# Optimization experiments

Hardware: AMD Instinct MI355X
Metric: run time of the kernel (lower is better)

The kernel has to match this reference:

```python
import jax, jax.numpy as jnp
import numpy as np

N, K, D, H, F = 4, 2048, 512, 8, 2048
Dh = D // H  # per-head dim_q = dim_v = dim_out = 64
EPS = 1e-10


def _uinit(k, shape, fan_sum):
    c = (6.0 / fan_sum) ** 0.5
    return jax.random.uniform(k, shape, jnp.float32, -c, c)


def setup_inputs() -> dict:
    key = jax.random.key(0)
    ks = jax.random.split(key, 8)
    x = jax.random.normal(ks[0], (N, K, D), jnp.float32)
    # per-head projection weights, stacked over heads: (H, D, Dh)
    Wq = _uinit(ks[1], (H, D, Dh), D + Dh)
    Wk = _uinit(ks[2], (H, D, Dh), D + Dh)
    Wv = _uinit(ks[3], (H, D, Dh), D + Dh)
    bq = jnp.zeros((H, Dh), jnp.float32)
    bk = jnp.zeros((H, Dh), jnp.float32)
    bv = jnp.zeros((H, Dh), jnp.float32)
    Wo = _uinit(ks[4], (H * Dh, D), H * Dh + D)
    bo = jnp.zeros((D,), jnp.float32)
    W1 = _uinit(ks[5], (D, F), D + F)
    b1 = jnp.zeros((F,), jnp.float32)
    W2 = _uinit(ks[6], (F, D), F + D)
    b2 = jnp.zeros((D,), jnp.float32)
    g1 = jnp.ones((D,), jnp.float32)
    be1 = jnp.zeros((D,), jnp.float32)
    g2 = jnp.ones((D,), jnp.float32)
    be2 = jnp.zeros((D,), jnp.float32)
    # causal mask: True = masked position (masked_fill semantics)
    mask = jnp.broadcast_to(jnp.triu(jnp.ones((K, K), bool), 1), (N, K, K))
    return dict(x=x, Wq=Wq, bq=bq, Wk=Wk, bk=bk, Wv=Wv, bv=bv, Wo=Wo, bo=bo,
                W1=W1, b1=b1, W2=W2, b2=b2, g1=g1, be1=be1, g2=g2, be2=be2,
                mask=mask)


def _layer_norm(x, g, b):
    m = x.mean(-1, keepdims=True)
    v = ((x - m) ** 2).mean(-1, keepdims=True)
    return g * (x - m) / jnp.sqrt(v + EPS) + b


def _block(x, Wq, bq, Wk, bk, Wv, bv, Wo, bo, W1, b1, W2, b2, g1, be1, g2, be2, mask):
    # per-head projections: (N, H, K, Dh)
    q = jnp.einsum('nkd,hde->nhke', x, Wq) + bq[None, :, None, :]
    k = jnp.einsum('nkd,hde->nhke', x, Wk) + bk[None, :, None, :]
    v = jnp.einsum('nkd,hde->nhke', x, Wv) + bv[None, :, None, :]
    # full score matrix (N, H, K, K) -- faithful to bmm-softmax-bmm
    s = jnp.einsum('nhqe,nhke->nhqk', q, k) / (Dh ** 0.5)
    s = jnp.where(mask[:, None], -1e9, s)
    w = jax.nn.softmax(s, axis=-1)
    att = jnp.einsum('nhqk,nhke->nhqe', w, v)
    att = att.transpose(0, 2, 1, 3).reshape(N, K, H * Dh)  # concat heads
    att = att @ Wo + bo
    h1 = _layer_norm(x + att, g1, be1)
    ff = jax.nn.relu(h1 @ W1 + b1) @ W2 + b2
    return _layer_norm(h1 + ff, g2, be2)


def reference(x, Wq, bq, Wk, bk, Wv, bv, Wo, bo, W1, b1, W2, b2, g1, be1, g2, be2, mask):
    return _block(x, Wq, bq, Wk, bk, Wv, bv, Wo, bo, W1, b1, W2, b2, g1, be1, g2, be2, mask)
```

## Files before the change

kernel.cpp:

```cpp
#include <hip/hip_runtime.h>
#include <cstdint>

typedef unsigned short u16;
typedef __bf16 bf16x8 __attribute__((ext_vector_type(8)));
typedef float f32x4 __attribute__((ext_vector_type(4)));
struct __align__(8) U2 { unsigned x, y; };

#define NEG_INF (-__builtin_inff())

__device__ __forceinline__ u16 f2bf(float f) {
  unsigned u = __builtin_bit_cast(unsigned, f);
  u += 0x7FFFu + ((u >> 16) & 1u);
  return (u16)(u >> 16);
}
__device__ __forceinline__ u16 bfbits(__bf16 x) { return __builtin_bit_cast(u16, x); }
__device__ __forceinline__ unsigned pk2(float a, float b) {
  u16 lo = bfbits((__bf16)a), hi = bfbits((__bf16)b);
  return (unsigned)lo | ((unsigned)hi << 16);
}

__device__ __forceinline__ void async16(u16* dst, const u16* src) {
  __builtin_amdgcn_global_load_lds(
      (__attribute__((address_space(1))) void*)(u16*)src,
      (__attribute__((address_space(3))) void*)dst, 16, 0, 0);
}

__global__ __launch_bounds__(256) void k_cvt(const float4* __restrict__ in,
                                             uint4* __restrict__ out, int n8) {
  int i = blockIdx.x * 256 + threadIdx.x;
  if (i >= n8) return;
  float4 a = in[2 * i], b = in[2 * i + 1];
  uint4 r;
  r.x = (unsigned)f2bf(a.x) | ((unsigned)f2bf(a.y) << 16);
  r.y = (unsigned)f2bf(a.z) | ((unsigned)f2bf(a.w) << 16);
  r.z = (unsigned)f2bf(b.x) | ((unsigned)f2bf(b.y) << 16);
  r.w = (unsigned)f2bf(b.z) | ((unsigned)f2bf(b.w) << 16);
  out[i] = r;
}

__global__ __launch_bounds__(256) void k_transpose(const float* __restrict__ in,
                                                   u16* __restrict__ out, int R, int C) {
  __shared__ float t[32][65];
  int b = blockIdx.z;
  int r0 = blockIdx.y * 32, c0 = blockIdx.x * 64;
  const float* ip = in + (size_t)b * R * C;
  u16* op = out + (size_t)b * R * C;
  int tx = threadIdx.x & 63, ty = threadIdx.x >> 6;
#pragma unroll
  for (int i = 0; i < 32; i += 4) {
    int r = r0 + ty + i, c = c0 + tx;
    t[ty + i][tx] = (r < R && c < C) ? ip[(size_t)r * C + c] : 0.f;
  }
  __syncthreads();
  int cx = threadIdx.x & 31, cy = threadIdx.x >> 5;
#pragma unroll
  for (int j = 0; j < 64; j += 8) {
    int oc = c0 + cy + j, orr = r0 + cx;
    if (oc < C && orr < R) op[(size_t)oc * R + orr] = f2bf(t[cx][cy + j]);
  }
}

__global__ __launch_bounds__(256) void k_transpose_qkv(const float* __restrict__ Wq,
                                                       const float* __restrict__ Wk,
                                                       const float* __restrict__ Wv,
                                                       u16* __restrict__ out) {
  __shared__ float t[32][65];
  int z = blockIdx.z;
  const float* W = (z < 8) ? Wq : (z < 16) ? Wk : Wv;
  const float* ip = W + (size_t)(z & 7) * 32768;
  u16* op = out + (size_t)z * 32768;
  int r0 = blockIdx.y * 32;
  int tx = threadIdx.x & 63, ty = threadIdx.x >> 6;
#pragma unroll
  for (int i = 0; i < 32; i += 4)
    t[ty + i][tx] = ip[(size_t)(r0 + ty + i) * 64 + tx];
  __syncthreads();
  int cx = threadIdx.x & 31, cy = threadIdx.x >> 5;
#pragma unroll
  for (int j = 0; j < 64; j += 8)
    op[(size_t)(cy + j) * 512 + r0 + cx] = f2bf(t[cx][cy + j]);
}

__global__ __launch_bounds__(256) void k_pack_bias(const float* __restrict__ bq,
                                                   const float* __restrict__ bk,
                                                   const float* __restrict__ bv,
                                                   float* __restrict__ bpk) {
  int i = blockIdx.x * 256 + threadIdx.x;
  if (i < 1536) {
    int m = i >> 9, r = i & 511;
    const float* B = (m == 0) ? bq : (m == 1) ? bk : bv;
    bpk[i] = B[r];
  }
}

template <int EPI, int BN>
__global__ __launch_bounds__(256) void k_gemm(const u16* __restrict__ A,
                                              const u16* __restrict__ BT,
                                              const float* __restrict__ bias,
                                              void* __restrict__ Cout,
                                              int M, int N, int Kd) {
  constexpr int HALF = 8192 + BN * 64;
  __shared__ __align__(16) u16 lds[2 * HALF];
  constexpr int NFR = BN / 32;
  constexpr int BITER = BN / 32;
  const int tid = threadIdx.x, wid = tid >> 6, lane = tid & 63;
  const int lr = lane & 15, lg = lane >> 4;
  const int wr = wid >> 1, wc = wid & 1;
  const int tm = blockIdx.x * 128, tn = blockIdx.y * BN;

  f32x4 acc[4][NFR] = {};

  const int srow = lane >> 3;
  const int kb = (lane & 7) ^ srow;

  auto STAGE = [&](int buf, int kt) {
    u16* base = lds + buf * HALF;
#pragma unroll
    for (int it = 0; it < 4; ++it) {
      int rid = wid * 4 + it;
      int row = rid * 8 + srow;
      async16(base + rid * 512, A + (size_t)(tm + row) * Kd + kt + kb * 8);
    }
#pragma unroll
    for (int it = 0; it < BITER; ++it) {
      int rid = wid * BITER + it;
      int row = rid * 8 + srow;
      async16(base + 8192 + rid * 512, BT + (size_t)(tn + row) * Kd + kt + kb * 8);
    }
  };

  const int nkt = Kd >> 6;
  STAGE(0, 0);
  __syncthreads();

  for (int ki = 0; ki < nkt; ++ki) {
    if (ki + 1 < nkt) STAGE((ki + 1) & 1, (ki + 1) << 6);
    const char* lp = (const char*)(lds + (ki & 1) * HALF);
#pragma unroll
    for (int ks = 0; ks < 2; ++ks) {
      const int kbyte = ks * 64 + lg * 16;
      bf16x8 af[4], bfr[NFR];
#pragma unroll
      for (int mi = 0; mi < 4; ++mi) {
        int row = wr * 64 + mi * 16 + lr;
        af[mi] = *(const bf16x8*)(lp + row * 128 + (kbyte ^ ((row & 7) << 4)));
      }
#pragma unroll
      for (int nj = 0; nj < NFR; ++nj) {
        int row = wc * (BN / 2) + nj * 16 + lr;
        bfr[nj] = *(const bf16x8*)(lp + 16384 + row * 128 + (kbyte ^ ((row & 7) << 4)));
      }
#pragma unroll
      for (int mi = 0; mi < 4; ++mi)
#pragma unroll
        for (int nj = 0; nj < NFR; ++nj)
          acc[mi][nj] = __builtin_amdgcn_mfma_f32_16x16x32_bf16(af[mi], bfr[nj], acc[mi][nj], 0, 0, 0);
    }
    __syncthreads();
  }

#pragma unroll
  for (int mi = 0; mi < 4; ++mi)
#pragma unroll
    for (int nj = 0; nj < NFR; ++nj) {
      int col = tn + wc * (BN / 2) + nj * 16 + lr;
      float bv = bias[col];
#pragma unroll
      for (int r = 0; r < 4; ++r) {
        int row = tm + wr * 64 + mi * 16 + lg * 4 + r;
        float v = acc[mi][nj][r] + bv;
        if (EPI == 1) v = v > 0.f ? v : 0.f;
        if (EPI == 2)
          ((float*)Cout)[(size_t)row * N + col] = v;
        else
          ((u16*)Cout)[(size_t)row * N + col] = f2bf(v);
      }
    }
}

__global__ __launch_bounds__(256) void k_attn(const u16* __restrict__ QKV,
                                              u16* __restrict__ att) {
  __shared__ __align__(16) u16 lds[36864];
  const int lin = blockIdx.x;
  const int L = (lin & 7) * 64 + (lin >> 3);
  const int p = L & 15, nh = L >> 4;
  const int n = nh >> 3, h = nh & 7;
  const int tid = threadIdx.x, wid = tid >> 6, lane = tid & 63;
  const int lr = lane & 15, lg = lane >> 4;
  char* lp = (char*)lds;
  const u16* Qp = QKV + (size_t)(n * 2048) * 1536 + h * 64;
  const u16* Kp = Qp + 512;
  const u16* Vp = Qp + 1024;

  const int vkv = (tid & 31) * 2;
  const int vd0 = (tid >> 5) * 8;
  const int pwb = 65536 + wid * 2048;
  const float C2 = 0.18033688011112042f;
  const float B0 = 14.426950408889634f;

  for (int ph = 0; ph < 2; ++ph) {
    const int qc = (ph == 0) ? p : 31 - p;
    const int ntiles = qc + 1;
    const int qw = qc * 64 + wid * 16;
    const int qa = qw + lr;

    bf16x8 qf[2];
#pragma unroll
    for (int ks = 0; ks < 2; ++ks)
      qf[ks] = *(const bf16x8*)(Qp + (size_t)(qw + lr) * 1536 + ks * 32 + lg * 8);

    f32x4 o[4] = {};
    float lpart = 0.f;

    auto STAGE_K = [&](int t, int b) {
      const int kv0 = t * 64;
#pragma unroll
      for (int it = 0; it < 2; ++it) {
        int c = (wid * 2 + it) * 64 + lane;
        int row = c >> 3, ce = ((c & 7) ^ (row & 7)) * 8;
        async16(&lds[b * 4096 + (wid * 2 + it) * 512],
                Kp + (size_t)(kv0 + row) * 1536 + ce);
      }
    };
    auto VLAND = [&](bf16x8 va, bf16x8 vb, int b) {
#pragma unroll
      for (int jj = 0; jj < 8; ++jj) {
        int d = vd0 + jj;
        unsigned pk = (unsigned)bfbits(va[jj]) | ((unsigned)bfbits(vb[jj]) << 16);
        *(unsigned*)(lp + 32768 + b * 8192 + d * 128 + ((vkv * 2) ^ ((d & 7) << 4))) = pk;
      }
    };
    auto COMPUTE = [&](int t, int b) {
      const int kv0 = t * 64;
      f32x4 s[4] = {};
      __builtin_amdgcn_s_setprio(1);
#pragma unroll
      for (int nj = 0; nj < 4; ++nj) {
        int row = nj * 16 + lr;
#pragma unroll
        for (int ks = 0; ks < 2; ++ks) {
          bf16x8 kf = *(const bf16x8*)(lp + b * 8192 + row * 128 +
                                       ((ks * 64 + lg * 16) ^ ((row & 7) << 4)));
          s[nj] = __builtin_amdgcn_mfma_f32_16x16x32_bf16(kf, qf[ks], s[nj], 0, 0, 0);
        }
      }
      __builtin_amdgcn_s_setprio(0);

      if (t == ntiles - 1) {
#pragma unroll
        for (int nj = 0; nj < 4; ++nj) {
          int kvb = kv0 + nj * 16 + lg * 4;
#pragma unroll
          for (int r = 0; r < 4; ++r)
            if (kvb + r > qa) s[nj][r] = NEG_INF;
        }
      }

      float psum = 0.f;
#pragma unroll
      for (int nj = 0; nj < 4; ++nj)
#pragma unroll
        for (int r = 0; r < 4; ++r) {
          float pv = exp2f(fmaf(s[nj][r], C2, -B0));
          s[nj][r] = pv;
          psum += pv;
        }
      lpart += psum;

#pragma unroll
      for (int nj = 0; nj < 4; ++nj) {
        U2 val;
        val.x = pk2(s[nj][0], s[nj][1]);
        val.y = pk2(s[nj][2], s[nj][3]);
        *(U2*)(lp + pwb + lr * 128 + ((nj * 32 + lg * 8) ^ ((lr & 7) << 4))) = val;
      }

      bf16x8 pa[2];
#pragma unroll
      for (int ks = 0; ks < 2; ++ks)
        pa[ks] = *(const bf16x8*)(lp + pwb + lr * 128 +
                                  ((ks * 64 + lg * 16) ^ ((lr & 7) << 4)));
      __builtin_amdgcn_s_setprio(1);
#pragma unroll
      for (int nd = 0; nd < 4; ++nd) {
        int row = nd * 16 + lr;
#pragma unroll
        for (int ks = 0; ks < 2; ++ks) {
          bf16x8 vf = *(const bf16x8*)(lp + 32768 + b * 8192 + row * 128 +
                                       ((ks * 64 + lg * 16) ^ ((row & 7) << 4)));
          o[nd] = __builtin_amdgcn_mfma_f32_16x16x32_bf16(vf, pa[ks], o[nd], 0, 0, 0);
        }
      }
      __builtin_amdgcn_s_setprio(0);
    };

    STAGE_K(0, 0);
    if (ntiles > 1) STAGE_K(1, 1);
    {
      bf16x8 v0 = *(const bf16x8*)(Vp + (size_t)vkv * 1536 + vd0);
      bf16x8 v1 = *(const bf16x8*)(Vp + (size_t)(vkv + 1) * 1536 + vd0);
      VLAND(v0, v1, 0);
      if (ntiles > 1) {
        bf16x8 v2 = *(const bf16x8*)(Vp + (size_t)(64 + vkv) * 1536 + vd0);
        bf16x8 v3 = *(const bf16x8*)(Vp + (size_t)(64 + vkv + 1) * 1536 + vd0);
        VLAND(v2, v3, 1);
      }
    }
    __syncthreads();

    for (int t = 0; t < ntiles; t += 2) {
      const bool pre0 = (t + 2 < ntiles);
      const bool pre1 = (t + 3 < ntiles);
      bf16x8 va0, vb0, va1, vb1;
      if (pre0) {
        STAGE_K(t + 2, (t + 2) & 3);
        va0 = *(const bf16x8*)(Vp + (size_t)((t + 2) * 64 + vkv) * 1536 + vd0);
        vb0 = *(const bf16x8*)(Vp + (size_t)((t + 2) * 64 + vkv + 1) * 1536 + vd0);
      }
      if (pre1) {
        STAGE_K(t + 3, (t + 3) & 3);
        va1 = *(const bf16x8*)(Vp + (size_t)((t + 3) * 64 + vkv) * 1536 + vd0);
        vb1 = *(const bf16x8*)(Vp + (size_t)((t + 3) * 64 + vkv + 1) * 1536 + vd0);
      }

      COMPUTE(t, t & 3);
      if (t + 1 < ntiles) COMPUTE(t + 1, (t + 1) & 3);

      if (pre0) VLAND(va0, vb0, (t + 2) & 3);
      if (pre1) VLAND(va1, vb1, (t + 3) & 3);
      __syncthreads();
    }

    float lsum = lpart;
    lsum += __shfl_xor(lsum, 16);
    lsum += __shfl_xor(lsum, 32);
    float li = 1.0f / lsum;

    u16* ap = att + (size_t)(n * 2048 + qw + lr) * 512 + h * 64 + lg * 4;
#pragma unroll
    for (int nd = 0; nd < 4; ++nd) {
      U2 val;
      val.x = pk2(o[nd][0] * li, o[nd][1] * li);
      val.y = pk2(o[nd][2] * li, o[nd][3] * li);
      *(U2*)(ap + nd * 16) = val;
    }
  }
}

__global__ __launch_bounds__(256) void k_add_ln(const float* __restrict__ X,
                                                const float* __restrict__ Y,
                                                const float* __restrict__ gam,
                                                const float* __restrict__ bet,
                                                float* __restrict__ outf,
                                                u16* __restrict__ outb) {
  const int wid = threadIdx.x >> 6, lane = threadIdx.x & 63;
  const size_t row = (size_t)blockIdx.x * 4 + wid;
  const float4* x = (const float4*)(X + row * 512);
  const float4* y = (const float4*)(Y + row * 512);
  float4 a0 = x[lane], a1 = x[lane + 64];
  float4 b0 = y[lane], b1 = y[lane + 64];
  float v[8];
  v[0] = a0.x + b0.x; v[1] = a0.y + b0.y; v[2] = a0.z + b0.z; v[3] = a0.w + b0.w;
  v[4] = a1.x + b1.x; v[5] = a1.y + b1.y; v[6] = a1.z + b1.z; v[7] = a1.w + b1.w;
  float s = 0.f, ss = 0.f;
#pragma unroll
  for (int i = 0; i < 8; ++i) { s += v[i]; ss += v[i] * v[i]; }
#pragma unroll
  for (int m = 1; m < 64; m <<= 1) { s += __shfl_xor(s, m); ss += __shfl_xor(ss, m); }
  float mean = s * (1.f / 512.f);
  float var = ss * (1.f / 512.f) - mean * mean;
  float rstd = rsqrtf(var + 1e-10f);
  float4 g0 = ((const float4*)gam)[lane], g1 = ((const float4*)gam)[lane + 64];
  float4 e0 = ((const float4*)bet)[lane], e1 = ((const float4*)bet)[lane + 64];
  float o[8];
  o[0] = g0.x * (v[0] - mean) * rstd + e0.x;
  o[1] = g0.y * (v[1] - mean) * rstd + e0.y;
  o[2] = g0.z * (v[2] - mean) * rstd + e0.z;
  o[3] = g0.w * (v[3] - mean) * rstd + e0.w;
  o[4] = g1.x * (v[4] - mean) * rstd + e1.x;
  o[5] = g1.y * (v[5] - mean) * rstd + e1.y;
  o[6] = g1.z * (v[6] - mean) * rstd + e1.z;
  o[7] = g1.w * (v[7] - mean) * rstd + e1.w;
  float4* of = (float4*)(outf + row * 512);
  float4 w0, w1;
  w0.x = o[0]; w0.y = o[1]; w0.z = o[2]; w0.w = o[3];
  w1.x = o[4]; w1.y = o[5]; w1.z = o[6]; w1.w = o[7];
  of[lane] = w0;
  of[lane + 64] = w1;
  if (outb) {
    u16* ob = outb + row * 512;
    U2 p0, p1;
    p0.x = pk2(o[0], o[1]); p0.y = pk2(o[2], o[3]);
    p1.x = pk2(o[4], o[5]); p1.y = pk2(o[6], o[7]);
    *(U2*)(ob + lane * 4) = p0;
    *(U2*)(ob + 256 + lane * 4) = p1;
  }
}

extern "C" void kernel_launch(void* const* d_in, const int* in_sizes, int n_in,
                              void* d_out, int out_size, void* d_ws, size_t ws_size,
                              hipStream_t stream) {
  const float* x  = (const float*)d_in[0];
  const float* Wq = (const float*)d_in[1];
  const float* bq = (const float*)d_in[2];
  const float* Wk = (const float*)d_in[3];
  const float* bk = (const float*)d_in[4];
  const float* Wv = (const float*)d_in[5];
  const float* bv = (const float*)d_in[6];
  const float* Wo = (const float*)d_in[7];
  const float* bo = (const float*)d_in[8];
  const float* W1 = (const float*)d_in[9];
  const float* b1 = (const float*)d_in[10];
  const float* W2 = (const float*)d_in[11];
  const float* b2 = (const float*)d_in[12];
  const float* g1 = (const float*)d_in[13];
  const float* be1 = (const float*)d_in[14];
  const float* g2 = (const float*)d_in[15];
  const float* be2 = (const float*)d_in[16];

  char* ws = (char*)d_ws;
  u16* xb   = (u16*)(ws + 0);
  u16* attb = (u16*)(ws + 0);
  u16* h1b  = (u16*)(ws + 0);
  u16* WqkvT = (u16*)(ws + (size_t)(8u << 20));
  u16* WoT = WqkvT + 786432;
  u16* W1T = WoT + 262144;
  u16* W2T = W1T + 1048576;
  float* bqkv = (float*)(W2T + 1048576);
  u16* QKV = (u16*)(ws + (size_t)(16u << 20));
  float* attproj = (float*)(ws + (size_t)(16u << 20));
  u16* ff1 = (u16*)(ws + (size_t)(16u << 20));
  float* ffn2 = (float*)(ws + (size_t)(50u << 20));
  float* h1f = (float*)d_out;

  k_cvt<<<2048, 256, 0, stream>>>((const float4*)x, (uint4*)xb, 524288);
  k_transpose_qkv<<<dim3(1, 16, 24), 256, 0, stream>>>(Wq, Wk, Wv, WqkvT);
  k_transpose<<<dim3(8, 16, 1), 256, 0, stream>>>(Wo, WoT, 512, 512);
  k_transpose<<<dim3(32, 16, 1), 256, 0, stream>>>(W1, W1T, 512, 2048);
  k_transpose<<<dim3(8, 64, 1), 256, 0, stream>>>(W2, W2T, 2048, 512);
  k_pack_bias<<<6, 256, 0, stream>>>(bq, bk, bv, bqkv);

  k_gemm<0, 128><<<dim3(64, 12), 256, 0, stream>>>(xb, WqkvT, bqkv, QKV, 8192, 1536, 512);
  k_attn<<<512, 256, 0, stream>>>(QKV, attb);
  k_gemm<2, 64><<<dim3(64, 8), 256, 0, stream>>>(attb, WoT, bo, attproj, 8192, 512, 512);
  k_add_ln<<<2048, 256, 0, stream>>>(x, attproj, g1, be1, h1f, h1b);
  k_gemm<1, 128><<<dim3(64, 16), 256, 0, stream>>>(h1b, W1T, b1, ff1, 8192, 2048, 512);
  k_gemm<2, 64><<<dim3(64, 8), 256, 0, stream>>>(ff1, W2T, b2, ffn2, 8192, 512, 2048);
  k_add_ln<<<2048, 256, 0, stream>>>(h1f, ffn2, g2, be2, (float*)d_out, nullptr);
}
```

Before: 179.1 us.

## Store GEMM residual outputs in bf16 and remap GEMM blocks for XCD locality

The Wo and W2 GEMMs now write bf16 instead of fp32 outputs, and the add+layernorm kernels read those bf16 values and widen them. This halves the write and read traffic of the two intermediate tensors, at a small cost in precision before the layer norm. GEMM grids become 1D, with block ids remapped so that the blocks landing on the same XCD cover a contiguous group of 8 M-tiles, which aims to improve L2 reuse of the A rows.

```diff
diff --git a/kernel.cpp b/kernel.cpp
--- a/kernel.cpp
+++ b/kernel.cpp
@@ -12,6 +12,10 @@
   unsigned u = __builtin_bit_cast(unsigned, f);
   u += 0x7FFFu + ((u >> 16) & 1u);
   return (u16)(u >> 16);
+}
+__device__ __forceinline__ float bf2f(u16 b) {
+  unsigned u = (unsigned)b << 16;
+  return __builtin_bit_cast(float, u);
 }
 __device__ __forceinline__ u16 bfbits(__bf16 x) { return __builtin_bit_cast(u16, x); }
 __device__ __forceinline__ unsigned pk2(float a, float b) {
@@ -97,7 +101,7 @@
 __global__ __launch_bounds__(256) void k_gemm(const u16* __restrict__ A,
                                               const u16* __restrict__ BT,
                                               const float* __restrict__ bias,
-                                              void* __restrict__ Cout,
+                                              u16* __restrict__ Cout,
                                               int M, int N, int Kd) {
   constexpr int HALF = 8192 + BN * 64;
   __shared__ __align__(16) u16 lds[2 * HALF];
@@ -106,7 +110,10 @@
   const int tid = threadIdx.x, wid = tid >> 6, lane = tid & 63;
   const int lr = lane & 15, lg = lane >> 4;
   const int wr = wid >> 1, wc = wid & 1;
-  const int tm = blockIdx.x * 128, tn = blockIdx.y * BN;
+  const int bid = blockIdx.x;
+  const int xcd = bid & 7, local = bid >> 3;
+  const int tm = (xcd * 8 + (local & 7)) * 128;
+  const int tn = (local >> 3) * BN;
 
   f32x4 acc[4][NFR] = {};
 
@@ -170,10 +177,7 @@
         int row = tm + wr * 64 + mi * 16 + lg * 4 + r;
         float v = acc[mi][nj][r] + bv;
         if (EPI == 1) v = v > 0.f ? v : 0.f;
-        if (EPI == 2)
-          ((float*)Cout)[(size_t)row * N + col] = v;
-        else
-          ((u16*)Cout)[(size_t)row * N + col] = f2bf(v);
+        Cout[(size_t)row * N + col] = f2bf(v);
       }
     }
 }
@@ -348,7 +352,7 @@
 }
 
 __global__ __launch_bounds__(256) void k_add_ln(const float* __restrict__ X,
-                                                const float* __restrict__ Y,
+                                                const u16* __restrict__ Yb,
                                                 const float* __restrict__ gam,
                                                 const float* __restrict__ bet,
                                                 float* __restrict__ outf,
@@ -356,12 +360,18 @@
   const int wid = threadIdx.x >> 6, lane = threadIdx.x & 63;
   const size_t row = (size_t)blockIdx.x * 4 + wid;
   const float4* x = (const float4*)(X + row * 512);
-  const float4* y = (const float4*)(Y + row * 512);
   float4 a0 = x[lane], a1 = x[lane + 64];
-  float4 b0 = y[lane], b1 = y[lane + 64];
+  U2 y0 = *(const U2*)(Yb + row * 512 + lane * 4);
+  U2 y1 = *(const U2*)(Yb + row * 512 + 256 + lane * 4);
   float v[8];
-  v[0] = a0.x + b0.x; v[1] = a0.y + b0.y; v[2] = a0.z + b0.z; v[3] = a0.w + b0.w;
-  v[4] = a1.x + b1.x; v[5] = a1.y + b1.y; v[6] = a1.z + b1.z; v[7] = a1.w + b1.w;
+  v[0] = a0.x + bf2f((u16)(y0.x & 0xFFFF));
+  v[1] = a0.y + bf2f((u16)(y0.x >> 16));
+  v[2] = a0.z + bf2f((u16)(y0.y & 0xFFFF));
+  v[3] = a0.w + bf2f((u16)(y0.y >> 16));
+  v[4] = a1.x + bf2f((u16)(y1.x & 0xFFFF));
+  v[5] = a1.y + bf2f((u16)(y1.x >> 16));
+  v[6] = a1.z + bf2f((u16)(y1.y & 0xFFFF));
+  v[7] = a1.w + bf2f((u16)(y1.y >> 16));
   float s = 0.f, ss = 0.f;
 #pragma unroll
   for (int i = 0; i < 8; ++i) { s += v[i]; ss += v[i] * v[i]; }
@@ -428,9 +438,9 @@
   u16* W2T = W1T + 1048576;
   float* bqkv = (float*)(W2T + 1048576);
   u16* QKV = (u16*)(ws + (size_t)(16u << 20));
-  float* attproj = (float*)(ws + (size_t)(16u << 20));
+  u16* attproj = (u16*)(ws + (size_t)(16u << 20));
   u16* ff1 = (u16*)(ws + (size_t)(16u << 20));
-  float* ffn2 = (float*)(ws + (size_t)(50u << 20));
+  u16* ffn2 = (u16*)(ws + (size_t)(50u << 20));
   float* h1f = (float*)d_out;
 
   k_cvt<<<2048, 256, 0, stream>>>((const float4*)x, (uint4*)xb, 524288);
@@ -440,11 +450,11 @@
   k_transpose<<<dim3(8, 64, 1), 256, 0, stream>>>(W2, W2T, 2048, 512);
   k_pack_bias<<<6, 256, 0, stream>>>(bq, bk, bv, bqkv);
 
-  k_gemm<0, 128><<<dim3(64, 12), 256, 0, stream>>>(xb, WqkvT, bqkv, QKV, 8192, 1536, 512);
+  k_gemm<0, 128><<<768, 256, 0, stream>>>(xb, WqkvT, bqkv, QKV, 8192, 1536, 512);
   k_attn<<<512, 256, 0, stream>>>(QKV, attb);
-  k_gemm<2, 64><<<dim3(64, 8), 256, 0, stream>>>(attb, WoT, bo, attproj, 8192, 512, 512);
+  k_gemm<0, 64><<<512, 256, 0, stream>>>(attb, WoT, bo, attproj, 8192, 512, 512);
   k_add_ln<<<2048, 256, 0, stream>>>(x, attproj, g1, be1, h1f, h1b);
-  k_gemm<1, 128><<<dim3(64, 16), 256, 0, stream>>>(h1b, W1T, b1, ff1, 8192, 2048, 512);
-  k_gemm<2, 64><<<dim3(64, 8), 256, 0, stream>>>(ff1, W2T, b2, ffn2, 8192, 512, 2048);
+  k_gemm<1, 128><<<1024, 256, 0, stream>>>(h1b, W1T, b1, ff1, 8192, 2048, 512);
+  k_gemm<0, 64><<<512, 256, 0, stream>>>(ff1, W2T, b2, ffn2, 8192, 512, 2048);
   k_add_ln<<<2048, 256, 0, stream>>>(h1f, ffn2, g2, be2, (float*)d_out, nullptr);
 }
```

After: 173.5 us. 3.1% less time.
